# Performance work log

Measured on AMD Instinct MI355X. Metric: run time of the kernel, lower is better.

The kernel has to match this reference:

```python
import jax, jax.numpy as jnp
import numpy as np
import math

L, B, T, E, HQ, HKV, V = 6, 4, 1024, 1024, 16, 4, 32000
D = E // HQ          # head dim = 64
G = HQ // HKV        # group size = 4
EKV = E // G         # kv proj dim = 256


def setup_inputs() -> dict:
    key = jax.random.key(0)
    ks = jax.random.split(key, 16)
    def n(k, shape):
        return jax.random.normal(k, shape, jnp.float32) * 0.02
    return dict(
        idx=jax.random.randint(ks[0], (B, T), 0, V),
        wte=n(ks[1], (V, E)),
        Wq=n(ks[2], (L, E, E)), bq=jnp.zeros((L, E), jnp.float32),
        Wk=n(ks[3], (L, EKV, E)), bk=jnp.zeros((L, EKV), jnp.float32),
        Wv=n(ks[4], (L, EKV, E)), bv=jnp.zeros((L, EKV), jnp.float32),
        Wo=n(ks[5], (L, E, E)), bo=jnp.zeros((L, E), jnp.float32),
        ln1_w=jnp.ones((L, E), jnp.float32), ln1_b=jnp.zeros((L, E), jnp.float32),
        ln2_w=jnp.ones((L, E), jnp.float32), ln2_b=jnp.zeros((L, E), jnp.float32),
        Wfc=n(ks[6], (L, 4 * E, E)), bfc=jnp.zeros((L, 4 * E), jnp.float32),
        Wproj=n(ks[7], (L, E, 4 * E)), bproj=jnp.zeros((L, E), jnp.float32),
        lnf_w=jnp.ones((E,), jnp.float32), lnf_b=jnp.zeros((E,), jnp.float32),
        lm_head=n(ks[8], (V, E)),
    )


def _ln(x, w, b):
    m = x.mean(-1, keepdims=True)
    v = ((x - m) ** 2).mean(-1, keepdims=True)
    return (x - m) * jax.lax.rsqrt(v + 1e-5) * w + b


def _gelu_new(x):
    c = math.sqrt(2.0 / math.pi)
    return 0.5 * x * (1.0 + jnp.tanh(c * (x + 0.044715 * x ** 3)))


def _rope_tables(t, d):
    # positions start at 1; thetas = base^(-2*(i-1)/d), i = 1..d/2
    pos = jnp.arange(1, t + 1, dtype=jnp.float32)
    thetas = 10000.0 ** (-2.0 * jnp.arange(d // 2, dtype=jnp.float32) / d)
    ang = pos[:, None] * thetas                      # [t, d/2]
    cos = jnp.concatenate([jnp.cos(ang)] * 2, -1)    # [t, d]
    sin = jnp.concatenate([jnp.sin(ang)] * 2, -1)
    return cos, sin


def _apply_rope(x, cos, sin):
    # x: [b, h, t, d]; x_cos = x; x_sin = concat(-right, left)
    x1, x2 = x[..., : D // 2], x[..., D // 2:]
    return x * cos + jnp.concatenate([-x2, x1], -1) * sin


def _gpt_forward(idx, wte, Wq, bq, Wk, bk, Wv, bv, Wo, bo,
                 ln1_w, ln1_b, ln2_w, ln2_b, Wfc, bfc, Wproj, bproj,
                 lnf_w, lnf_b, lm_head):
    cos, sin = _rope_tables(T, D)
    mask = jnp.tril(jnp.ones((T, T), bool))          # causal
    scale = 1.0 / math.sqrt(D)
    x = wte[idx]                                     # [B, T, E]
    for l in range(L):
        h = _ln(x, ln1_w[l], ln1_b[l])
        q = (h @ Wq[l].T + bq[l]).reshape(B, T, HQ, D).transpose(0, 2, 1, 3)
        k = (h @ Wk[l].T + bk[l]).reshape(B, T, HKV, D).transpose(0, 2, 1, 3)
        v = (h @ Wv[l].T + bv[l]).reshape(B, T, HKV, D).transpose(0, 2, 1, 3)
        q = _apply_rope(q, cos, sin)
        k = _apply_rope(k, cos, sin)
        q = q.reshape(B, HKV, G, T, D)               # kv-major head grouping
        att = jnp.einsum('bhgqd,bhkd->bhgqk', q, k) * scale
        att = jnp.where(mask, att, -jnp.inf)
        att = jax.nn.softmax(att, axis=-1)
        y = jnp.einsum('bhgqk,bhkd->bhgqd', att, v)
        y = y.transpose(0, 3, 1, 2, 4).reshape(B, T, E)   # b q (h g d)
        x = x + (y @ Wo[l].T + bo[l])
        h2 = _ln(x, ln2_w[l], ln2_b[l])
        ff = _gelu_new(h2 @ Wfc[l].T + bfc[l]) @ Wproj[l].T + bproj[l]
        x = x + ff
    x = _ln(x, lnf_w, lnf_b)
    return x @ lm_head.T                             # [B, T, V] logits


def reference(idx, wte, Wq, bq, Wk, bk, Wv, bv, Wo, bo,
              ln1_w, ln1_b, ln2_w, ln2_b, Wfc, bfc, Wproj, bproj,
              lnf_w, lnf_b, lm_head):
    return _gpt_forward(idx, wte, Wq, bq, Wk, bk, Wv, bv, Wo, bo,
                        ln1_w, ln1_b, ln2_w, ln2_b, Wfc, bfc, Wproj, bproj,
                        lnf_w, lnf_b, lm_head)
```

## Files before the change

kernel.cpp:

```cpp
#include <hip/hip_runtime.h>

#define Lz 6
#define Bz 4
#define Tz 1024
#define Ez 1024
#define HQz 16
#define HKVz 4
#define Dz 64
#define EKVz 256
#define Vz 32000
#define FFz 4096
#define QKVz 1536

typedef __attribute__((ext_vector_type(4))) float f32x4;
typedef __attribute__((ext_vector_type(8))) short short8;
typedef unsigned short ushort_t;

__device__ inline ushort_t f2b(float f) {
  union { float f; unsigned u; } x; x.f = f;
  unsigned r = x.u + 0x7fffu + ((x.u >> 16) & 1u);
  return (ushort_t)(r >> 16);
}
__device__ inline float b2f(ushort_t u) {
  union { unsigned u; float f; } x; x.u = ((unsigned)u) << 16;
  return x.f;
}
__device__ inline unsigned packbf(float lo, float hi) {
  return (unsigned)f2b(lo) | ((unsigned)f2b(hi) << 16);
}

__device__ inline void gload16(const void* g, void* l) {
  __builtin_amdgcn_global_load_lds(
      (const __attribute__((address_space(1))) void*)g,
      (__attribute__((address_space(3))) void*)l, 16, 0, 0);
}

template<int BIAS, int GELU, int WF32>
__global__ __launch_bounds__(512, 2) void gemm_bt256(
    const ushort_t* __restrict__ A, const ushort_t* __restrict__ Bw,
    const float* __restrict__ bias,
    float* __restrict__ Cf, ushort_t* __restrict__ Cb,
    int M, int N, int K)
{
  __shared__ ushort_t sA[2][2][128 * 64];
  __shared__ ushort_t sB[2][2][128 * 64];
  const int tid = threadIdx.x;
  const int lane = tid & 63, wid = tid >> 6;
  const int wr = wid >> 2, wc = wid & 3;
  const int l15 = lane & 15, l4 = lane >> 4;

  const int gx = gridDim.x;
  const int nwg = gx * gridDim.y;
  const int orig = blockIdx.y * gx + blockIdx.x;
  const int qq = nwg >> 3, rr = nwg & 7;
  const int xcd = orig & 7, loc = orig >> 3;
  const int swz = (xcd < rr) ? (xcd * (qq + 1) + loc)
                             : (rr * (qq + 1) + (xcd - rr) * qq + loc);
  const int bm = swz % gx, bn = swz / gx;

  const int NT = K >> 6;

  auto stage = [&](const ushort_t* src, int row_base, int k0, ushort_t* dst) {
#pragma unroll
    for (int i = 0; i < 2; ++i) {
      int s = i * 512 + tid;
      int row = s >> 3, jp = s & 7;
      int jlog = jp ^ (row & 7);
      gload16(src + (size_t)(row_base + row) * K + k0 + jlog * 8, (char*)dst + s * 16);
    }
  };

  stage(A,  bm * 256,       0, &sA[0][0][0]);
  stage(A,  bm * 256 + 128, 0, &sA[0][1][0]);
  stage(Bw, bn * 256,       0, &sB[0][0][0]);
  stage(Bw, bn * 256 + 128, 0, &sB[0][1][0]);
  stage(A,  bm * 256,       64, &sA[1][0][0]);
  stage(A,  bm * 256 + 128, 64, &sA[1][1][0]);
  stage(Bw, bn * 256,       64, &sB[1][0][0]);
  stage(Bw, bn * 256 + 128, 64, &sB[1][1][0]);
  asm volatile("s_waitcnt vmcnt(8)" ::: "memory");
  __builtin_amdgcn_sched_barrier(0);
  __builtin_amdgcn_s_barrier();
  __builtin_amdgcn_sched_barrier(0);

  f32x4 acc[8][4] = {};
  const int axc = l15 & 7;

  for (int t = 0; t < NT; ++t) {
    const int b = t & 1;
    const ushort_t* pA = &sA[b][wr][0];
    const ushort_t* pB = &sB[b][wc >> 1][(wc & 1) * 64 * 64];
    short8 aF[8][2], bF[4][2];

#pragma unroll
    for (int mt = 0; mt < 4; ++mt)
#pragma unroll
      for (int ks = 0; ks < 2; ++ks)
        aF[mt][ks] = *(const short8*)&pA[(mt * 16 + l15) * 64 + (((ks << 2) + l4) ^ axc) * 8];
#pragma unroll
    for (int nt = 0; nt < 4; ++nt)
      bF[nt][0] = *(const short8*)&pB[(nt * 16 + l15) * 64 + (l4 ^ axc) * 8];
    __builtin_amdgcn_s_setprio(1);
#pragma unroll
    for (int mt = 0; mt < 4; ++mt)
#pragma unroll
      for (int nt = 0; nt < 4; ++nt)
        acc[mt][nt] = __builtin_amdgcn_mfma_f32_16x16x32_bf16(aF[mt][0], bF[nt][0], acc[mt][nt], 0, 0, 0);
    __builtin_amdgcn_s_setprio(0);

#pragma unroll
    for (int mt = 4; mt < 8; ++mt)
#pragma unroll
      for (int ks = 0; ks < 2; ++ks)
        aF[mt][ks] = *(const short8*)&pA[(mt * 16 + l15) * 64 + (((ks << 2) + l4) ^ axc) * 8];
#pragma unroll
    for (int nt = 0; nt < 4; ++nt)
      bF[nt][1] = *(const short8*)&pB[(nt * 16 + l15) * 64 + ((4 + l4) ^ axc) * 8];
    __builtin_amdgcn_s_setprio(1);
#pragma unroll
    for (int mt = 0; mt < 4; ++mt)
#pragma unroll
      for (int nt = 0; nt < 4; ++nt)
        acc[mt][nt] = __builtin_amdgcn_mfma_f32_16x16x32_bf16(aF[mt][1], bF[nt][1], acc[mt][nt], 0, 0, 0);
    __builtin_amdgcn_s_setprio(0);

    asm volatile("s_waitcnt lgkmcnt(0)" ::: "memory");
    __builtin_amdgcn_sched_barrier(0);
    __builtin_amdgcn_s_barrier();
    __builtin_amdgcn_sched_barrier(0);

    const bool pf = (t + 2 < NT);
    if (pf) {
      const int k2 = (t + 2) << 6;
      stage(Bw, bn * 256,       k2, &sB[b][0][0]);
      stage(Bw, bn * 256 + 128, k2, &sB[b][1][0]);
    }
    __builtin_amdgcn_s_setprio(1);
#pragma unroll
    for (int mt = 4; mt < 8; ++mt)
#pragma unroll
      for (int nt = 0; nt < 4; ++nt)
        acc[mt][nt] = __builtin_amdgcn_mfma_f32_16x16x32_bf16(aF[mt][0], bF[nt][0], acc[mt][nt], 0, 0, 0);
    __builtin_amdgcn_s_setprio(0);

    if (pf) {
      const int k2 = (t + 2) << 6;
      stage(A, bm * 256,       k2, &sA[b][0][0]);
      stage(A, bm * 256 + 128, k2, &sA[b][1][0]);
    }
    __builtin_amdgcn_s_setprio(1);
#pragma unroll
    for (int mt = 4; mt < 8; ++mt)
#pragma unroll
      for (int nt = 0; nt < 4; ++nt)
        acc[mt][nt] = __builtin_amdgcn_mfma_f32_16x16x32_bf16(aF[mt][1], bF[nt][1], acc[mt][nt], 0, 0, 0);
    __builtin_amdgcn_s_setprio(0);

    if (t + 1 < NT) {
      if (pf) { asm volatile("s_waitcnt vmcnt(8)" ::: "memory"); }
      else    { asm volatile("s_waitcnt vmcnt(0)" ::: "memory"); }
      __builtin_amdgcn_sched_barrier(0);
      __builtin_amdgcn_s_barrier();
      __builtin_amdgcn_sched_barrier(0);
    }
  }

#pragma unroll
  for (int mt = 0; mt < 8; ++mt) {
#pragma unroll
    for (int nt = 0; nt < 4; ++nt) {
      const int col = bn * 256 + wc * 64 + nt * 16 + l15;
#pragma unroll
      for (int i = 0; i < 4; ++i) {
        const int row = bm * 256 + wr * 128 + mt * 16 + l4 * 4 + i;
        float v = acc[mt][nt][i];
        if (BIAS) v += bias[col];
        if (GELU) {
          float x = v;
          v = 0.5f * x * (1.f + tanhf(0.7978845608028654f * (x + 0.044715f * x * x * x)));
        }
        const size_t o = (size_t)row * N + col;
        if (WF32) Cf[o] = v; else Cb[o] = f2b(v);
      }
    }
  }
}

template<int BIAS, int RES, int GELU, int WBF16, int ROPE>
__global__ __launch_bounds__(256) void gemm_bt64(
    const ushort_t* __restrict__ A, const ushort_t* __restrict__ Bw,
    const float* __restrict__ bias, const ushort_t* __restrict__ res,
    ushort_t* __restrict__ Cb, ushort_t* __restrict__ vtb,
    const float2* __restrict__ tab,
    int M, int N, int K)
{
  __shared__ ushort_t sA[2][128 * 32];
  __shared__ ushort_t sB[2][64 * 32];
  const int tid = threadIdx.x;
  const int lane = tid & 63, wid = tid >> 6;
  const int l15 = lane & 15, l4 = lane >> 4;

  const int gx = gridDim.x;
  const int nwg = gx * gridDim.y;
  const int orig = blockIdx.y * gx + blockIdx.x;
  const int qq = nwg >> 3, rr = nwg & 7;
  const int xcd = orig & 7, loc = orig >> 3;
  const int swz = (xcd < rr) ? (xcd * (qq + 1) + loc)
                             : (rr * (qq + 1) + (xcd - rr) * qq + loc);
  const int bm = swz % gx, bn = swz / gx;

  f32x4 acc[2][4] = {};
  const int nK = K >> 5;

#pragma unroll
  for (int j = 0; j < 2; ++j) {
    int s = wid * 128 + j * 64 + lane;
    int row = s >> 2, c8 = (s & 3) << 3;
    gload16(A + (size_t)(bm * 128 + row) * K + c8, (char*)&sA[0][0] + s * 16);
  }
  {
    int s = wid * 64 + lane;
    int row = s >> 2, c8 = (s & 3) << 3;
    gload16(Bw + (size_t)(bn * 64 + row) * K + c8, (char*)&sB[0][0] + s * 16);
  }
  __syncthreads();

  int cur = 0;
  for (int kt = 0; kt < nK; ++kt) {
    if (kt + 1 < nK) {
      const int k0 = (kt + 1) << 5;
      const int nb = cur ^ 1;
#pragma unroll
      for (int j = 0; j < 2; ++j) {
        int s = wid * 128 + j * 64 + lane;
        int row = s >> 2, c8 = (s & 3) << 3;
        gload16(A + (size_t)(bm * 128 + row) * K + k0 + c8, (char*)&sA[nb][0] + s * 16);
      }
      {
        int s = wid * 64 + lane;
        int row = s >> 2, c8 = (s & 3) << 3;
        gload16(Bw + (size_t)(bn * 64 + row) * K + k0 + c8, (char*)&sB[nb][0] + s * 16);
      }
    }
    short8 aF[2], bF[4];
#pragma unroll
    for (int mt = 0; mt < 2; ++mt)
      aF[mt] = *(const short8*)&sA[cur][(wid * 32 + mt * 16 + l15) * 32 + l4 * 8];
#pragma unroll
    for (int nt = 0; nt < 4; ++nt)
      bF[nt] = *(const short8*)&sB[cur][(nt * 16 + l15) * 32 + l4 * 8];
#pragma unroll
    for (int mt = 0; mt < 2; ++mt)
#pragma unroll
      for (int nt = 0; nt < 4; ++nt)
        acc[mt][nt] = __builtin_amdgcn_mfma_f32_16x16x32_bf16(aF[mt], bF[nt], acc[mt][nt], 0, 0, 0);
    __syncthreads();
    cur ^= 1;
  }

  if (ROPE) {
    const int col0 = bn * 64;
    const bool isv = (col0 >= 1280);
#pragma unroll
    for (int mt = 0; mt < 2; ++mt) {
      const int row_base = bm * 128 + wid * 32 + mt * 16 + l4 * 4;
      const int bb = row_base >> 10, t0 = row_base & (Tz - 1);
      if (isv) {
#pragma unroll
        for (int nt = 0; nt < 4; ++nt) {
          const int col = col0 + nt * 16 + l15;
          const int cm = col - 1280, hk = cm >> 6, d = cm & 63;
          ushort4 w;
          w.x = f2b(acc[mt][nt][0] + bias[col]);
          w.y = f2b(acc[mt][nt][1] + bias[col]);
          w.z = f2b(acc[mt][nt][2] + bias[col]);
          w.w = f2b(acc[mt][nt][3] + bias[col]);
          *(ushort4*)&vtb[((size_t)(bb * HKVz + hk) * 64 + d) * Tz + t0] = w;
        }
      } else {
#pragma unroll
        for (int i = 0; i < 4; ++i) {
          const int row = row_base + i;
          const int t = row & (Tz - 1);
#pragma unroll
          for (int nt = 0; nt < 2; ++nt) {
            const int col = col0 + nt * 16 + l15;
            const int jj = nt * 16 + l15;
            const float2 cs = tab[t * 32 + jj];
            const float x1 = acc[mt][nt][i] + bias[col];
            const float x2 = acc[mt][nt + 2][i] + bias[col + 32];
            Cb[(size_t)row * N + col]      = f2b(x1 * cs.x - x2 * cs.y);
            Cb[(size_t)row * N + col + 32] = f2b(x2 * cs.x + x1 * cs.y);
          }
        }
      }
    }
    return;
  }

#pragma unroll
  for (int mt = 0; mt < 2; ++mt) {
#pragma unroll
    for (int nt = 0; nt < 4; ++nt) {
      const int col = bn * 64 + nt * 16 + l15;
#pragma unroll
      for (int i = 0; i < 4; ++i) {
        const int row = bm * 128 + wid * 32 + mt * 16 + l4 * 4 + i;
        float v = acc[mt][nt][i];
        if (BIAS) v += bias[col];
        if (GELU) {
          float t = v;
          v = 0.5f * t * (1.f + tanhf(0.7978845608028654f * (t + 0.044715f * t * t * t)));
        }
        const size_t o = (size_t)row * N + col;
        if (RES) v += b2f(res[o]);
        if (WBF16) Cb[o] = f2b(v);
      }
    }
  }
}

__global__ __launch_bounds__(256, 4) void attn_k(
    const ushort_t* __restrict__ qkv, const ushort_t* __restrict__ vt,
    ushort_t* __restrict__ y)
{
  __shared__ ushort_t sK[2][64 * 64];
  __shared__ ushort_t sV[2][64 * 64];
  __shared__ unsigned sPu[4][512];
  const int bh = blockIdx.y;
  const int b = bh >> 4, h = bh & 15, hk = h >> 2;
  const int tid = threadIdx.x, lane = tid & 63, wid = tid >> 6;
  const int l15 = lane & 15, l4 = lane >> 4;
  const int xr = l15 & 7;

  for (int pass = 0; pass < 2; ++pass) {
    const int qt = pass ? (int)blockIdx.x : (Tz / 64 - 1 - (int)blockIdx.x);
    const int qrow0 = qt * 64 + wid * 16;
    const int qg = qrow0 + l15;
    const int ntile = qt + 1;

    short8 aQ[2];
#pragma unroll
    for (int ks = 0; ks < 2; ++ks)
      aQ[ks] = *(const short8*)&qkv[(size_t)(b * Tz + qrow0 + l15) * QKVz + h * 64 + ks * 32 + l4 * 8];

    float m = -1e30f, lsum = 0.f;
    f32x4 o[4] = {};

    if (pass) __syncthreads();

#pragma unroll
    for (int j = 0; j < 2; ++j) {
      int s = wid * 128 + j * 64 + lane;
      int row = s >> 3, jp = s & 7, jlog = jp ^ (row & 7);
      gload16(qkv + (size_t)(b * Tz + row) * QKVz + Ez + hk * 64 + jlog * 8, (char*)&sK[0][0] + s * 16);
      gload16(vt + (size_t)((b * HKVz + hk) * 64 + row) * Tz + jlog * 8, (char*)&sV[0][0] + s * 16);
    }

    for (int t = 0; t < ntile; ++t) {
      asm volatile("s_waitcnt vmcnt(0)" ::: "memory");
      __syncthreads();
      if (t + 1 < ntile) {
        const int nb = (t + 1) & 1;
#pragma unroll
        for (int j = 0; j < 2; ++j) {
          int s = wid * 128 + j * 64 + lane;
          int row = s >> 3, jp = s & 7, jlog = jp ^ (row & 7);
          gload16(qkv + (size_t)(b * Tz + (t + 1) * 64 + row) * QKVz + Ez + hk * 64 + jlog * 8,
                  (char*)&sK[nb][0] + s * 16);
          gload16(vt + (size_t)((b * HKVz + hk) * 64 + row) * Tz + (t + 1) * 64 + jlog * 8,
                  (char*)&sV[nb][0] + s * 16);
        }
      }
      const ushort_t* K = &sK[t & 1][0];
      const ushort_t* V = &sV[t & 1][0];

      f32x4 sacc[4] = {};
#pragma unroll
      for (int nt = 0; nt < 4; ++nt) {
#pragma unroll
        for (int ks = 0; ks < 2; ++ks) {
          short8 aK = *(const short8*)&K[(nt * 16 + l15) * 64 + (((ks << 2) + l4) ^ xr) * 8];
          sacc[nt] = __builtin_amdgcn_mfma_f32_16x16x32_bf16(aK, aQ[ks], sacc[nt], 0, 0, 0);
        }
      }

      float sv[4][4];
      float pmax = -1e30f;
#pragma unroll
      for (int nt = 0; nt < 4; ++nt)
#pragma unroll
        for (int i = 0; i < 4; ++i) {
          int key = t * 64 + nt * 16 + l4 * 4 + i;
          float s = sacc[nt][i] * 0.125f;
          if (key > qg) s = -1e30f;
          sv[nt][i] = s;
          pmax = fmaxf(pmax, s);
        }
      pmax = fmaxf(pmax, __shfl_xor(pmax, 16));
      pmax = fmaxf(pmax, __shfl_xor(pmax, 32));
      const float mnew = fmaxf(m, pmax);
      const float corr = __expf(m - mnew);
      float psum = 0.f;
#pragma unroll
      for (int nt = 0; nt < 4; ++nt)
#pragma unroll
        for (int i = 0; i < 4; ++i) {
          float p = __expf(sv[nt][i] - mnew);
          sv[nt][i] = p;
          psum += p;
        }
      psum += __shfl_xor(psum, 16);
      psum += __shfl_xor(psum, 32);
      lsum = lsum * corr + psum;
      m = mnew;
#pragma unroll
      for (int dt = 0; dt < 4; ++dt) o[dt] *= corr;

#pragma unroll
      for (int nt = 0; nt < 4; ++nt) {
        uint2 u;
        u.x = packbf(sv[nt][0], sv[nt][1]);
        u.y = packbf(sv[nt][2], sv[nt][3]);
        *(uint2*)&sPu[wid][l15 * 32 + (((nt * 2 + (l4 >> 1)) ^ xr) << 2) + ((l4 & 1) << 1)] = u;
      }
      short8 aP[2];
#pragma unroll
      for (int ks = 0; ks < 2; ++ks)
        aP[ks] = *(const short8*)&sPu[wid][l15 * 32 + ((((ks << 2) + l4) ^ xr) << 2)];

#pragma unroll
      for (int dt = 0; dt < 4; ++dt) {
#pragma unroll
        for (int ks = 0; ks < 2; ++ks) {
          short8 aV = *(const short8*)&V[(dt * 16 + l15) * 64 + (((ks << 2) + l4) ^ xr) * 8];
          o[dt] = __builtin_amdgcn_mfma_f32_16x16x32_bf16(aV, aP[ks], o[dt], 0, 0, 0);
        }
      }
    }

    const float inv = 1.f / lsum;
    const size_t yrow = (size_t)(b * Tz + qrow0 + l15) * Ez + h * 64;
#pragma unroll
    for (int dt = 0; dt < 4; ++dt) {
      ushort4 w;
      w.x = f2b(o[dt][0] * inv);
      w.y = f2b(o[dt][1] * inv);
      w.z = f2b(o[dt][2] * inv);
      w.w = f2b(o[dt][3] * inv);
      *(ushort4*)&y[yrow + dt * 16 + l4 * 4] = w;
    }
  }
}

__global__ __launch_bounds__(256) void ln_bf16(
    const ushort_t* __restrict__ x, const float* __restrict__ w,
    const float* __restrict__ b, ushort_t* __restrict__ out)
{
  __shared__ float red[8];
  const int row = blockIdx.x, tid = threadIdx.x;
  ushort4 xv = *(const ushort4*)&x[(size_t)row * Ez + tid * 4];
  float v0 = b2f(xv.x), v1 = b2f(xv.y), v2 = b2f(xv.z), v3 = b2f(xv.w);
  float s = v0 + v1 + v2 + v3;
  float sq = v0 * v0 + v1 * v1 + v2 * v2 + v3 * v3;
#pragma unroll
  for (int off = 1; off < 64; off <<= 1) { s += __shfl_xor(s, off); sq += __shfl_xor(sq, off); }
  if ((tid & 63) == 0) { red[(tid >> 6) * 2] = s; red[(tid >> 6) * 2 + 1] = sq; }
  __syncthreads();
  const float ts = red[0] + red[2] + red[4] + red[6];
  const float tq = red[1] + red[3] + red[5] + red[7];
  const float mean = ts * (1.f / Ez);
  const float var = tq * (1.f / Ez) - mean * mean;
  const float rstd = rsqrtf(var + 1e-5f);
  float4 wv = *(const float4*)&w[tid * 4];
  float4 bv = *(const float4*)&b[tid * 4];
  ushort4 ov;
  ov.x = f2b((v0 - mean) * rstd * wv.x + bv.x);
  ov.y = f2b((v1 - mean) * rstd * wv.y + bv.y);
  ov.z = f2b((v2 - mean) * rstd * wv.z + bv.z);
  ov.w = f2b((v3 - mean) * rstd * wv.w + bv.w);
  *(ushort4*)&out[(size_t)row * Ez + tid * 4] = ov;
}

__global__ __launch_bounds__(256) void embed_k(
    const int* __restrict__ idx, const float* __restrict__ wte, ushort_t* __restrict__ x)
{
  int i = blockIdx.x * 256 + threadIdx.x;
  int row = i >> 8, c = (i & 255) << 2;
  float4 v = *(const float4*)&wte[(size_t)idx[row] * Ez + c];
  ushort4 o;
  o.x = f2b(v.x); o.y = f2b(v.y); o.z = f2b(v.z); o.w = f2b(v.w);
  *(ushort4*)&x[(size_t)row * Ez + c] = o;
}

__global__ __launch_bounds__(256) void cvt_bf16(
    const float* __restrict__ in, ushort_t* __restrict__ out, int n)
{
  int i = (blockIdx.x * 256 + threadIdx.x) * 4;
  if (i >= n) return;
  float4 v = *(const float4*)&in[i];
  ushort4 o;
  o.x = f2b(v.x); o.y = f2b(v.y); o.z = f2b(v.z); o.w = f2b(v.w);
  *(ushort4*)&out[i] = o;
}

__global__ __launch_bounds__(256) void cvt_layer(
    const float* __restrict__ Wq, const float* __restrict__ Wk,
    const float* __restrict__ Wv, const float* __restrict__ Wo_,
    const float* __restrict__ Wfc_, const float* __restrict__ Wpj_,
    ushort_t* __restrict__ wqkv, ushort_t* __restrict__ wo,
    ushort_t* __restrict__ wfc, ushort_t* __restrict__ wpj)
{
  int i = (blockIdx.x * 256 + threadIdx.x) * 4;
  const float* src; ushort_t* dst; int off;
  if (i < 1048576)       { src = Wq;   dst = wqkv;           off = i; }
  else if (i < 1310720)  { src = Wk;   dst = wqkv + 1048576; off = i - 1048576; }
  else if (i < 1572864)  { src = Wv;   dst = wqkv + 1310720; off = i - 1310720; }
  else if (i < 2621440)  { src = Wo_;  dst = wo;             off = i - 1572864; }
  else if (i < 6815744)  { src = Wfc_; dst = wfc;            off = i - 2621440; }
  else                   { src = Wpj_; dst = wpj;            off = i - 6815744; }
  float4 v = *(const float4*)&src[off];
  ushort4 o;
  o.x = f2b(v.x); o.y = f2b(v.y); o.z = f2b(v.z); o.w = f2b(v.w);
  *(ushort4*)&dst[off] = o;
}

__global__ __launch_bounds__(256) void rope_tab_k(float2* __restrict__ tab)
{
  int i = blockIdx.x * 256 + threadIdx.x;
  int t = i >> 5, j = i & 31;
  float theta = powf(10000.0f, -(float)j / 32.0f);
  float ang = (float)(t + 1) * theta;
  tab[i] = make_float2(cosf(ang), sinf(ang));
}

__global__ __launch_bounds__(256) void biascat_all(
    const float* __restrict__ bq, const float* __restrict__ bk,
    const float* __restrict__ bv, float* __restrict__ out)
{
  int i = blockIdx.x * 256 + threadIdx.x;
  int l = i / QKVz, j = i - l * QKVz;
  float v = (j < Ez) ? bq[l * Ez + j]
          : ((j < Ez + EKVz) ? bk[l * EKVz + j - Ez] : bv[l * EKVz + j - Ez - EKVz]);
  out[i] = v;
}

template<int BIAS, int RES, int GELU, int WBF16, int ROPE = 0>
static void launch_gemm64(const ushort_t* A, const ushort_t* Bw, const float* bias,
                          const ushort_t* res, ushort_t* Cb,
                          ushort_t* vtb, const float* tab,
                          int M, int N, int K, hipStream_t s)
{
  dim3 g(M / 128, N / 64);
  gemm_bt64<BIAS, RES, GELU, WBF16, ROPE><<<g, 256, 0, s>>>(
      A, Bw, bias, res, Cb, vtb, (const float2*)tab, M, N, K);
}

extern "C" void kernel_launch(void* const* d_in, const int* in_sizes, int n_in,
                              void* d_out, int out_size, void* d_ws, size_t ws_size,
                              hipStream_t stream)
{
  (void)in_sizes; (void)n_in; (void)out_size; (void)ws_size;
  const int*   idx   = (const int*)d_in[0];
  const float* wte   = (const float*)d_in[1];
  const float* Wq    = (const float*)d_in[2];
  const float* bq    = (const float*)d_in[3];
  const float* Wk    = (const float*)d_in[4];
  const float* bk    = (const float*)d_in[5];
  const float* Wv    = (const float*)d_in[6];
  const float* bv    = (const float*)d_in[7];
  const float* Wo    = (const float*)d_in[8];
  const float* bo    = (const float*)d_in[9];
  const float* ln1w  = (const float*)d_in[10];
  const float* ln1b  = (const float*)d_in[11];
  const float* ln2w  = (const float*)d_in[12];
  const float* ln2b  = (const float*)d_in[13];
  const float* Wfc   = (const float*)d_in[14];
  const float* bfc   = (const float*)d_in[15];
  const float* Wproj = (const float*)d_in[16];
  const float* bproj = (const float*)d_in[17];
  const float* lnfw  = (const float*)d_in[18];
  const float* lnfb  = (const float*)d_in[19];
  const float* lmh   = (const float*)d_in[20];
  float* out = (float*)d_out;

  char* ws = (char*)d_ws;
  size_t off = 0;
  auto alloc = [&](size_t bytes) -> void* {
    void* p = ws + off;
    off += (bytes + 255) & ~(size_t)255;
    return p;
  };
  ushort_t* wbuf  = (ushort_t*)alloc((size_t)Vz * Ez * 2);
  ushort_t* x     = (ushort_t*)alloc((size_t)Bz * Tz * Ez * 2);
  ushort_t* hb    = (ushort_t*)alloc((size_t)Bz * Tz * Ez * 2);
  ushort_t* qkvb  = (ushort_t*)alloc((size_t)Bz * Tz * QKVz * 2);
  ushort_t* vtb   = (ushort_t*)alloc((size_t)Bz * HKVz * 64 * Tz * 2);
  ushort_t* yb    = (ushort_t*)alloc((size_t)Bz * Tz * Ez * 2);
  ushort_t* ffb   = (ushort_t*)alloc((size_t)Bz * Tz * FFz * 2);
  float*    tab   = (float*)alloc((size_t)Tz * 32 * 2 * 4);
  float*    qbia  = (float*)alloc((size_t)Lz * QKVz * 4);

  ushort_t* wqkv = wbuf;
  ushort_t* wo   = wqkv + (size_t)QKVz * Ez;
  ushort_t* wfc  = wo + (size_t)Ez * Ez;
  ushort_t* wpj  = wfc + (size_t)FFz * Ez;

  const int M = Bz * Tz;

  rope_tab_k<<<Tz * 32 / 256, 256, 0, stream>>>((float2*)tab);
  biascat_all<<<Lz * QKVz / 256, 256, 0, stream>>>(bq, bk, bv, qbia);
  embed_k<<<Bz * Tz, 256, 0, stream>>>(idx, wte, x);

  for (int l = 0; l < Lz; ++l) {
    ln_bf16<<<M, 256, 0, stream>>>(x, ln1w + l * Ez, ln1b + l * Ez, hb);
    cvt_layer<<<10752, 256, 0, stream>>>(
        Wq + (size_t)l * Ez * Ez, Wk + (size_t)l * EKVz * Ez, Wv + (size_t)l * EKVz * Ez,
        Wo + (size_t)l * Ez * Ez, Wfc + (size_t)l * FFz * Ez, Wproj + (size_t)l * Ez * FFz,
        wqkv, wo, wfc, wpj);
    launch_gemm64<1, 0, 0, 1, 1>(hb, wqkv, qbia + l * QKVz, nullptr, qkvb, vtb, tab,
                                 M, QKVz, Ez, stream);
    attn_k<<<dim3(Tz / 128, Bz * HQz), 256, 0, stream>>>(qkvb, vtb, yb);
    launch_gemm64<1, 1, 0, 1>(yb, wo, bo + l * Ez, x, x, nullptr, nullptr,
                              M, Ez, Ez, stream);
    ln_bf16<<<M, 256, 0, stream>>>(x, ln2w + l * Ez, ln2b + l * Ez, hb);
    {
      dim3 g(M / 256, FFz / 256);
      gemm_bt256<1, 1, 0><<<g, 512, 0, stream>>>(hb, wfc, bfc + l * FFz, nullptr, ffb, M, FFz, Ez);
    }
    launch_gemm64<1, 1, 0, 1>(ffb, wpj, bproj + l * Ez, x, x, nullptr, nullptr,
                              M, Ez, FFz, stream);
  }
  ln_bf16<<<M, 256, 0, stream>>>(x, lnfw, lnfb, hb);
  cvt_bf16<<<(Vz * Ez / 4 + 255) / 256, 256, 0, stream>>>(lmh, wbuf, Vz * Ez);
  {
    dim3 g(M / 256, Vz / 256);
    gemm_bt256<0, 0, 1><<<g, 512, 0, stream>>>(hb, wbuf, nullptr, out, nullptr, M, Vz, Ez);
  }
}
```

Baseline: 1.703 ms.

## Raise wave priority around MFMA blocks, merge setup kernels, use gemm64 for FC

Wraps the MFMA sequences in the GEMM and attention kernels with s_setprio raise/lower so that waves in their math phase get issue priority over waves doing loads. Merges the rope-table and bias-concat setup kernels into one launch. Switches the FC GEMM (N=4096) from the 256x256 tile kernel to the 128x64 tile kernel with GELU enabled, which gives more blocks but less reuse per tile.

```diff
diff --git a/kernel.cpp b/kernel.cpp
--- a/kernel.cpp
+++ b/kernel.cpp
@@ -249,11 +249,13 @@
 #pragma unroll
     for (int nt = 0; nt < 4; ++nt)
       bF[nt] = *(const short8*)&sB[cur][(nt * 16 + l15) * 32 + l4 * 8];
+    __builtin_amdgcn_s_setprio(1);
 #pragma unroll
     for (int mt = 0; mt < 2; ++mt)
 #pragma unroll
       for (int nt = 0; nt < 4; ++nt)
         acc[mt][nt] = __builtin_amdgcn_mfma_f32_16x16x32_bf16(aF[mt], bF[nt], acc[mt][nt], 0, 0, 0);
+    __builtin_amdgcn_s_setprio(0);
     __syncthreads();
     cur ^= 1;
   }
@@ -376,6 +378,7 @@
       const ushort_t* V = &sV[t & 1][0];
 
       f32x4 sacc[4] = {};
+      __builtin_amdgcn_s_setprio(1);
 #pragma unroll
       for (int nt = 0; nt < 4; ++nt) {
 #pragma unroll
@@ -384,6 +387,7 @@
           sacc[nt] = __builtin_amdgcn_mfma_f32_16x16x32_bf16(aK, aQ[ks], sacc[nt], 0, 0, 0);
         }
       }
+      __builtin_amdgcn_s_setprio(0);
 
       float sv[4][4];
       float pmax = -1e30f;
@@ -429,6 +433,7 @@
       for (int ks = 0; ks < 2; ++ks)
         aP[ks] = *(const short8*)&sPu[wid][l15 * 32 + ((((ks << 2) + l4) ^ xr) << 2)];
 
+      __builtin_amdgcn_s_setprio(1);
 #pragma unroll
       for (int dt = 0; dt < 4; ++dt) {
 #pragma unroll
@@ -437,6 +442,7 @@
           o[dt] = __builtin_amdgcn_mfma_f32_16x16x32_bf16(aV, aP[ks], o[dt], 0, 0, 0);
         }
       }
+      __builtin_amdgcn_s_setprio(0);
     }
 
     const float inv = 1.f / lsum;
@@ -525,24 +531,21 @@
   *(ushort4*)&dst[off] = o;
 }
 
-__global__ __launch_bounds__(256) void rope_tab_k(float2* __restrict__ tab)
+__global__ __launch_bounds__(256) void setup_k(
+    const float* __restrict__ bq, const float* __restrict__ bk,
+    const float* __restrict__ bv, float2* __restrict__ tab, float* __restrict__ qbia)
 {
   int i = blockIdx.x * 256 + threadIdx.x;
   int t = i >> 5, j = i & 31;
   float theta = powf(10000.0f, -(float)j / 32.0f);
   float ang = (float)(t + 1) * theta;
   tab[i] = make_float2(cosf(ang), sinf(ang));
-}
-
-__global__ __launch_bounds__(256) void biascat_all(
-    const float* __restrict__ bq, const float* __restrict__ bk,
-    const float* __restrict__ bv, float* __restrict__ out)
-{
-  int i = blockIdx.x * 256 + threadIdx.x;
-  int l = i / QKVz, j = i - l * QKVz;
-  float v = (j < Ez) ? bq[l * Ez + j]
-          : ((j < Ez + EKVz) ? bk[l * EKVz + j - Ez] : bv[l * EKVz + j - Ez - EKVz]);
-  out[i] = v;
+  if (i < Lz * QKVz) {
+    int l = i / QKVz, jj = i - l * QKVz;
+    float v = (jj < Ez) ? bq[l * Ez + jj]
+            : ((jj < Ez + EKVz) ? bk[l * EKVz + jj - Ez] : bv[l * EKVz + jj - Ez - EKVz]);
+    qbia[i] = v;
+  }
 }
 
 template<int BIAS, int RES, int GELU, int WBF16, int ROPE = 0>
@@ -608,8 +611,7 @@
 
   const int M = Bz * Tz;
 
-  rope_tab_k<<<Tz * 32 / 256, 256, 0, stream>>>((float2*)tab);
-  biascat_all<<<Lz * QKVz / 256, 256, 0, stream>>>(bq, bk, bv, qbia);
+  setup_k<<<Tz * 32 / 256, 256, 0, stream>>>(bq, bk, bv, (float2*)tab, qbia);
   embed_k<<<Bz * Tz, 256, 0, stream>>>(idx, wte, x);
 
   for (int l = 0; l < Lz; ++l) {
@@ -624,10 +626,8 @@
     launch_gemm64<1, 1, 0, 1>(yb, wo, bo + l * Ez, x, x, nullptr, nullptr,
                               M, Ez, Ez, stream);
     ln_bf16<<<M, 256, 0, stream>>>(x, ln2w + l * Ez, ln2b + l * Ez, hb);
-    {
-      dim3 g(M / 256, FFz / 256);
-      gemm_bt256<1, 1, 0><<<g, 512, 0, stream>>>(hb, wfc, bfc + l * FFz, nullptr, ffb, M, FFz, Ez);
-    }
+    launch_gemm64<1, 0, 1, 1>(hb, wfc, bfc + l * FFz, nullptr, ffb, nullptr, nullptr,
+                              M, FFz, Ez, stream);
     launch_gemm64<1, 1, 0, 1>(ffb, wpj, bproj + l * Ez, x, x, nullptr, nullptr,
                               M, Ez, FFz, stream);
   }
```

New measurement: 1.819 ms. +6.8%, slower.
